# Performance work log

Hardware: AMD Instinct MI355X
Metric: run time of the kernel (lower is better)

Reference implementation:

```python
import jax, jax.numpy as jnp
import numpy as np

B, K, D, C = 16384, 8, 128, 128


def setup_inputs() -> dict:
    key = jax.random.key(0)
    k1, k2, k3, k4, k5 = jax.random.split(key, 5)
    return {
        "graph_embeddings": jax.random.normal(k1, (B, D), dtype=jnp.float32),
        "retrieval_embeddings": jax.random.normal(k2, (B, K, D), dtype=jnp.float32),
        "W_adapter": jax.random.normal(k3, (D, D), dtype=jnp.float32) / np.sqrt(D),
        "W_pred": jax.random.normal(k4, (D, C), dtype=jnp.float32) / np.sqrt(D),
        "b_pred": jnp.zeros((C,), dtype=jnp.float32),
        "labels": jax.random.randint(k5, (B, K), 0, C, dtype=jnp.int64).astype(jnp.int32),
    }


def reference(graph_embeddings, retrieval_embeddings, W_adapter, W_pred, b_pred, labels):
    # g_label = Softmax(dim=1)(graph_pred_linear(graph_embeddings))   [B, C]
    g_label = jax.nn.softmax(graph_embeddings @ W_pred + b_pred, axis=1)

    # concat_H = cat([graph_embeddings] + retrievals, -1).view(B, K+1, D)
    concat_H = jnp.concatenate([graph_embeddings[:, None, :], retrieval_embeddings], axis=1)  # [B, K+1, D]

    # adapter: bilinear attention scores, softmax over the K+1 candidates
    scores = jnp.einsum("bd,de,bme->bm", graph_embeddings, W_adapter, concat_H)  # [B, K+1]
    attention = jax.nn.softmax(scores, axis=1)

    # generic-dataset branch of the per-sample loop, vectorized:
    #   adjusted[b] = attn[b,0] * g_label[b]
    #   adjusted[b, labels[b,k]] += attn[b, k]   for k in range(K)
    # (note: faithful to the original, which indexes attention[b][k], not k+1)
    one_hot = jax.nn.one_hot(labels, C, dtype=g_label.dtype)  # [B, K, C]
    adjusted_label = attention[:, :1] * g_label + jnp.einsum("bk,bkc->bc", attention[:, :K], one_hot)
    return adjusted_label
```

## Files before the change

kernel.cpp:

```cpp
#include <hip/hip_runtime.h>


#define SB      32
#define THREADS 256

__global__ __launch_bounds__(THREADS)
void graph_retrieval_fused(const float* __restrict__ G,
                           const float* __restrict__ R,
                           const float* __restrict__ Wa,
                           const float* __restrict__ Wp,
                           const float* __restrict__ bp,
                           const int*   __restrict__ labels,
                           float* __restrict__ out)
{
    __shared__ float g_lds[SB * 128];
    __shared__ float logit_lds[SB * 132];
    __shared__ float t_lds[SB * 128];
    __shared__ float attn_lds[SB * 12];
    __shared__ float stat_m[SB], stat_iz[SB];
    __shared__ int   lab_lds[SB * 8];

    const int tid = threadIdx.x;
    const int b0  = blockIdx.x * SB;

    {
        const float4* Gv  = (const float4*)(G + (size_t)b0 * 128);
        float4*       gl4 = (float4*)g_lds;
        #pragma unroll
        for (int j = 0; j < 4; ++j)
            gl4[j * 256 + tid] = Gv[j * 256 + tid];
        lab_lds[tid] = labels[b0 * 8 + tid];
    }
    __syncthreads();

    const int c     = tid & 127;
    const int h     = tid >> 7;
    const int sbase = h * 16;

    float t_acc[16], l_acc[16];
    {
        const float bias = bp[c];
        #pragma unroll
        for (int i = 0; i < 16; ++i) { t_acc[i] = 0.f; l_acc[i] = bias; }

        for (int d0 = 0; d0 < 128; d0 += 4) {
            const float wa0 = Wa[(d0 + 0) * 128 + c];
            const float wa1 = Wa[(d0 + 1) * 128 + c];
            const float wa2 = Wa[(d0 + 2) * 128 + c];
            const float wa3 = Wa[(d0 + 3) * 128 + c];
            const float wp0 = Wp[(d0 + 0) * 128 + c];
            const float wp1 = Wp[(d0 + 1) * 128 + c];
            const float wp2 = Wp[(d0 + 2) * 128 + c];
            const float wp3 = Wp[(d0 + 3) * 128 + c];
            #pragma unroll
            for (int i = 0; i < 16; ++i) {
                const float4 g4 = *(const float4*)&g_lds[(sbase + i) * 128 + d0];
                t_acc[i] += g4.x * wa0 + g4.y * wa1 + g4.z * wa2 + g4.w * wa3;
                l_acc[i] += g4.x * wp0 + g4.y * wp1 + g4.z * wp2 + g4.w * wp3;
            }
        }

        #pragma unroll
        for (int i = 0; i < 16; ++i) {
            t_lds[(sbase + i) * 128 + c]     = t_acc[i];
            logit_lds[(sbase + i) * 132 + c] = l_acc[i];
        }
    }
    __syncthreads();

    {
        const int s = tid >> 3;
        const int p = tid & 7;
        const float* row = &logit_lds[s * 132 + p * 16];
        float mx = row[0];
        #pragma unroll
        for (int j = 1; j < 16; ++j) mx = fmaxf(mx, row[j]);
        #pragma unroll
        for (int off = 1; off < 8; off <<= 1)
            mx = fmaxf(mx, __shfl_xor(mx, off, 64));
        float sum = 0.f;
        #pragma unroll
        for (int j = 0; j < 16; ++j) sum += __expf(row[j] - mx);
        #pragma unroll
        for (int off = 1; off < 8; off <<= 1)
            sum += __shfl_xor(sum, off, 64);
        if (p == 0) { stat_m[s] = mx; stat_iz[s] = 1.f / sum; }
    }
    __syncthreads();

    {
        const int wv   = tid >> 6;
        const int lane = tid & 63;
        #pragma unroll
        for (int si = 0; si < 8; ++si) {
            const int s = wv * 8 + si;
            const float2 t2 = *(const float2*)&t_lds[s * 128 + 2 * lane];
            float sc[9];
            {
                const float2 g2 = *(const float2*)&g_lds[s * 128 + 2 * lane];
                sc[0] = t2.x * g2.x + t2.y * g2.y;
            }
            const float2* Rrow = (const float2*)(R + (size_t)(b0 + s) * 8 * 128);
            #pragma unroll
            for (int m = 1; m < 9; ++m) {
                const float2 hv = Rrow[(m - 1) * 64 + lane];
                sc[m] = t2.x * hv.x + t2.y * hv.y;
            }
            #pragma unroll
            for (int off = 32; off > 0; off >>= 1) {
                #pragma unroll
                for (int m = 0; m < 9; ++m)
                    sc[m] += __shfl_xor(sc[m], off, 64);
            }
            float mx = sc[0];
            #pragma unroll
            for (int m = 1; m < 9; ++m) mx = fmaxf(mx, sc[m]);
            float e[9], sum = 0.f;
            #pragma unroll
            for (int m = 0; m < 9; ++m) { e[m] = __expf(sc[m] - mx); sum += e[m]; }
            const float inv = 1.f / sum;
            if (lane == 0) {
                #pragma unroll
                for (int m = 0; m < 9; ++m) attn_lds[s * 12 + m] = e[m] * inv;
            }
        }
    }
    __syncthreads();

    #pragma unroll
    for (int i = 0; i < 16; ++i) {
        const int s = sbase + i;
        const float gl  = __expf(l_acc[i] - stat_m[s]) * stat_iz[s];
        float val = attn_lds[s * 12 + 0] * gl;
        #pragma unroll
        for (int k = 0; k < 8; ++k)
            val += (lab_lds[s * 8 + k] == c) ? attn_lds[s * 12 + k] : 0.f;
        out[(size_t)(b0 + s) * 128 + c] = val;
    }
}

extern "C" void kernel_launch(void* const* d_in, const int* in_sizes, int n_in,
                              void* d_out, int out_size, void* d_ws, size_t ws_size,
                              hipStream_t stream) {
    const float* G      = (const float*)d_in[0];
    const float* R      = (const float*)d_in[1];
    const float* Wa     = (const float*)d_in[2];
    const float* Wp     = (const float*)d_in[3];
    const float* bpred  = (const float*)d_in[4];
    const int*   labels = (const int*)d_in[5];
    float*       o      = (float*)d_out;

    const int B = in_sizes[0] / 128;
    dim3 grid(B / SB), block(THREADS);
    hipLaunchKernelGGL(graph_retrieval_fused, grid, block, 0, stream,
                       G, R, Wa, Wp, bpred, labels, o);
}
```

Before: 139.0 us.

## Shrink per-block sample tile to 8 and merge softmax stats into attention phase

Reduces samples per block from 32 to 8, which gives four times as many blocks, smaller LDS use and fewer accumulators per thread, aiming for higher occupancy and better latency hiding of the retrieval-embedding loads. The logit softmax statistics are now computed by each wave for its two samples with 64-lane shuffles inside the attention phase, which removes one barrier. Each wave interleaves two samples' score reductions for more instruction-level parallelism. The cost is that every block re-reads both 128x128 weight matrices for only 8 samples, so weight traffic per sample rises fourfold, mostly served from L2.

After: 137.0 us. Within noise of the previous version (-1.4%).

```diff
diff --git a/kernel.cpp b/kernel.cpp
--- a/kernel.cpp
+++ b/kernel.cpp
@@ -1,7 +1,7 @@
 #include <hip/hip_runtime.h>
 
 
-#define SB      32
+#define SB      8
 #define THREADS 256
 
 __global__ __launch_bounds__(THREADS)
@@ -14,54 +14,48 @@
                            float* __restrict__ out)
 {
     __shared__ float g_lds[SB * 128];
+    __shared__ float t_lds[SB * 128];
     __shared__ float logit_lds[SB * 132];
-    __shared__ float t_lds[SB * 128];
-    __shared__ float attn_lds[SB * 12];
+    __shared__ float attn_lds[SB * 8];
     __shared__ float stat_m[SB], stat_iz[SB];
     __shared__ int   lab_lds[SB * 8];
 
     const int tid = threadIdx.x;
     const int b0  = blockIdx.x * SB;
 
-    {
-        const float4* Gv  = (const float4*)(G + (size_t)b0 * 128);
-        float4*       gl4 = (float4*)g_lds;
-        #pragma unroll
-        for (int j = 0; j < 4; ++j)
-            gl4[j * 256 + tid] = Gv[j * 256 + tid];
-        lab_lds[tid] = labels[b0 * 8 + tid];
-    }
+    ((float4*)g_lds)[tid] = ((const float4*)(G + (size_t)b0 * 128))[tid];
+    if (tid < SB * 8) lab_lds[tid] = labels[b0 * 8 + tid];
     __syncthreads();
 
     const int c     = tid & 127;
     const int h     = tid >> 7;
-    const int sbase = h * 16;
+    const int sbase = h * 4;
 
-    float t_acc[16], l_acc[16];
+    float t_acc[4], l_acc[4];
     {
         const float bias = bp[c];
         #pragma unroll
-        for (int i = 0; i < 16; ++i) { t_acc[i] = 0.f; l_acc[i] = bias; }
+        for (int i = 0; i < 4; ++i) { t_acc[i] = 0.f; l_acc[i] = bias; }
 
-        for (int d0 = 0; d0 < 128; d0 += 4) {
-            const float wa0 = Wa[(d0 + 0) * 128 + c];
-            const float wa1 = Wa[(d0 + 1) * 128 + c];
-            const float wa2 = Wa[(d0 + 2) * 128 + c];
-            const float wa3 = Wa[(d0 + 3) * 128 + c];
-            const float wp0 = Wp[(d0 + 0) * 128 + c];
-            const float wp1 = Wp[(d0 + 1) * 128 + c];
-            const float wp2 = Wp[(d0 + 2) * 128 + c];
-            const float wp3 = Wp[(d0 + 3) * 128 + c];
+        for (int d0 = 0; d0 < 128; d0 += 8) {
+            float wa[8], wp8[8];
             #pragma unroll
-            for (int i = 0; i < 16; ++i) {
-                const float4 g4 = *(const float4*)&g_lds[(sbase + i) * 128 + d0];
-                t_acc[i] += g4.x * wa0 + g4.y * wa1 + g4.z * wa2 + g4.w * wa3;
-                l_acc[i] += g4.x * wp0 + g4.y * wp1 + g4.z * wp2 + g4.w * wp3;
+            for (int j = 0; j < 8; ++j) {
+                wa[j]  = Wa[(d0 + j) * 128 + c];
+                wp8[j] = Wp[(d0 + j) * 128 + c];
+            }
+            #pragma unroll
+            for (int i = 0; i < 4; ++i) {
+                const float4 ga = *(const float4*)&g_lds[(sbase + i) * 128 + d0];
+                const float4 gb = *(const float4*)&g_lds[(sbase + i) * 128 + d0 + 4];
+                t_acc[i] += ga.x * wa[0] + ga.y * wa[1] + ga.z * wa[2] + ga.w * wa[3]
+                          + gb.x * wa[4] + gb.y * wa[5] + gb.z * wa[6] + gb.w * wa[7];
+                l_acc[i] += ga.x * wp8[0] + ga.y * wp8[1] + ga.z * wp8[2] + ga.w * wp8[3]
+                          + gb.x * wp8[4] + gb.y * wp8[5] + gb.z * wp8[6] + gb.w * wp8[7];
             }
         }
-
         #pragma unroll
-        for (int i = 0; i < 16; ++i) {
+        for (int i = 0; i < 4; ++i) {
             t_lds[(sbase + i) * 128 + c]     = t_acc[i];
             logit_lds[(sbase + i) * 132 + c] = l_acc[i];
         }
@@ -69,72 +63,84 @@
     __syncthreads();
 
     {
-        const int s = tid >> 3;
-        const int p = tid & 7;
-        const float* row = &logit_lds[s * 132 + p * 16];
-        float mx = row[0];
-        #pragma unroll
-        for (int j = 1; j < 16; ++j) mx = fmaxf(mx, row[j]);
-        #pragma unroll
-        for (int off = 1; off < 8; off <<= 1)
-            mx = fmaxf(mx, __shfl_xor(mx, off, 64));
-        float sum = 0.f;
-        #pragma unroll
-        for (int j = 0; j < 16; ++j) sum += __expf(row[j] - mx);
-        #pragma unroll
-        for (int off = 1; off < 8; off <<= 1)
-            sum += __shfl_xor(sum, off, 64);
-        if (p == 0) { stat_m[s] = mx; stat_iz[s] = 1.f / sum; }
-    }
-    __syncthreads();
-
-    {
         const int wv   = tid >> 6;
         const int lane = tid & 63;
+        const int s0   = wv * 2;
+
+        const float2 e0 = *(const float2*)&logit_lds[s0 * 132 + 2 * lane];
+        const float2 e1 = *(const float2*)&logit_lds[(s0 + 1) * 132 + 2 * lane];
+        float m0 = fmaxf(e0.x, e0.y), m1 = fmaxf(e1.x, e1.y);
         #pragma unroll
-        for (int si = 0; si < 8; ++si) {
-            const int s = wv * 8 + si;
-            const float2 t2 = *(const float2*)&t_lds[s * 128 + 2 * lane];
-            float sc[9];
-            {
-                const float2 g2 = *(const float2*)&g_lds[s * 128 + 2 * lane];
-                sc[0] = t2.x * g2.x + t2.y * g2.y;
-            }
-            const float2* Rrow = (const float2*)(R + (size_t)(b0 + s) * 8 * 128);
+        for (int off = 32; off > 0; off >>= 1) {
+            m0 = fmaxf(m0, __shfl_xor(m0, off, 64));
+            m1 = fmaxf(m1, __shfl_xor(m1, off, 64));
+        }
+        float z0 = __expf(e0.x - m0) + __expf(e0.y - m0);
+        float z1 = __expf(e1.x - m1) + __expf(e1.y - m1);
+        #pragma unroll
+        for (int off = 32; off > 0; off >>= 1) {
+            z0 += __shfl_xor(z0, off, 64);
+            z1 += __shfl_xor(z1, off, 64);
+        }
+        if (lane == 0) {
+            stat_m[s0]      = m0;  stat_iz[s0]      = 1.f / z0;
+            stat_m[s0 + 1]  = m1;  stat_iz[s0 + 1]  = 1.f / z1;
+        }
+
+        float scA[9], scB[9];
+        {
+            const float2 tA = *(const float2*)&t_lds[s0 * 128 + 2 * lane];
+            const float2 tB = *(const float2*)&t_lds[(s0 + 1) * 128 + 2 * lane];
+            const float2 gA = *(const float2*)&g_lds[s0 * 128 + 2 * lane];
+            const float2 gB = *(const float2*)&g_lds[(s0 + 1) * 128 + 2 * lane];
+            scA[0] = tA.x * gA.x + tA.y * gA.y;
+            scB[0] = tB.x * gB.x + tB.y * gB.y;
+            const float2* RrA = (const float2*)(R + (size_t)(b0 + s0) * 8 * 128);
+            const float2* RrB = (const float2*)(R + (size_t)(b0 + s0 + 1) * 8 * 128);
             #pragma unroll
             for (int m = 1; m < 9; ++m) {
-                const float2 hv = Rrow[(m - 1) * 64 + lane];
-                sc[m] = t2.x * hv.x + t2.y * hv.y;
+                const float2 ra = RrA[(m - 1) * 64 + lane];
+                const float2 rb = RrB[(m - 1) * 64 + lane];
+                scA[m] = tA.x * ra.x + tA.y * ra.y;
+                scB[m] = tB.x * rb.x + tB.y * rb.y;
             }
+        }
+        #pragma unroll
+        for (int off = 32; off > 0; off >>= 1) {
             #pragma unroll
-            for (int off = 32; off > 0; off >>= 1) {
-                #pragma unroll
-                for (int m = 0; m < 9; ++m)
-                    sc[m] += __shfl_xor(sc[m], off, 64);
+            for (int m = 0; m < 9; ++m) {
+                scA[m] += __shfl_xor(scA[m], off, 64);
+                scB[m] += __shfl_xor(scB[m], off, 64);
             }
-            float mx = sc[0];
+        }
+        float mxA = scA[0], mxB = scB[0];
+        #pragma unroll
+        for (int m = 1; m < 9; ++m) { mxA = fmaxf(mxA, scA[m]); mxB = fmaxf(mxB, scB[m]); }
+        float eA[9], eB[9], sA = 0.f, sB = 0.f;
+        #pragma unroll
+        for (int m = 0; m < 9; ++m) {
+            eA[m] = __expf(scA[m] - mxA); sA += eA[m];
+            eB[m] = __expf(scB[m] - mxB); sB += eB[m];
+        }
+        const float iA = 1.f / sA, iB = 1.f / sB;
+        if (lane == 0) {
             #pragma unroll
-            for (int m = 1; m < 9; ++m) mx = fmaxf(mx, sc[m]);
-            float e[9], sum = 0.f;
-            #pragma unroll
-            for (int m = 0; m < 9; ++m) { e[m] = __expf(sc[m] - mx); sum += e[m]; }
-            const float inv = 1.f / sum;
-            if (lane == 0) {
-                #pragma unroll
-                for (int m = 0; m < 9; ++m) attn_lds[s * 12 + m] = e[m] * inv;
+            for (int m = 0; m < 8; ++m) {
+                attn_lds[s0 * 8 + m]       = eA[m] * iA;
+                attn_lds[(s0 + 1) * 8 + m] = eB[m] * iB;
             }
         }
     }
     __syncthreads();
 
     #pragma unroll
-    for (int i = 0; i < 16; ++i) {
+    for (int i = 0; i < 4; ++i) {
         const int s = sbase + i;
-        const float gl  = __expf(l_acc[i] - stat_m[s]) * stat_iz[s];
-        float val = attn_lds[s * 12 + 0] * gl;
+        const float gl = __expf(l_acc[i] - stat_m[s]) * stat_iz[s];
+        float val = attn_lds[s * 8 + 0] * gl;
         #pragma unroll
         for (int k = 0; k < 8; ++k)
-            val += (lab_lds[s * 8 + k] == c) ? attn_lds[s * 12 + k] : 0.f;
+            val += (lab_lds[s * 8 + k] == c) ? attn_lds[s * 8 + k] : 0.f;
         out[(size_t)(b0 + s) * 128 + c] = val;
     }
 }
```

## Compute G×[Wa|Wp] with split-bf16 MFMA and prepacked weight fragments

Applied to the files above, without the earlier changes.

Replaces the scalar FP32 projection loop with bf16 MFMA 16x16x32 instructions, using a hi/lo bf16 split (three MFMAs per tile) to approximate FP32 accuracy. A small pre-kernel packs Wa and Wp into MFMA B-fragment layout in the workspace on every call. Also halves rows per block to 16, pads LDS rows, and fuses the logit softmax stats with the attention-score phase to remove one barrier. This trades some precision (truncated bf16 split) and an extra launch for less scalar FMA work.

Measured after the change: 120.1 us. -13.6%, faster.

```diff
diff --git a/kernel.cpp b/kernel.cpp
--- a/kernel.cpp
+++ b/kernel.cpp
@@ -1,141 +1,226 @@
 #include <hip/hip_runtime.h>
 
 
-#define SB      32
+#define SB      16
 #define THREADS 256
 
-__global__ __launch_bounds__(THREADS)
+typedef __attribute__((ext_vector_type(8))) short bfrag_t;
+typedef __attribute__((ext_vector_type(4))) float facc_t;
+
+__device__ __forceinline__ unsigned short bf16_hi_trunc(float f) {
+    return (unsigned short)(__builtin_bit_cast(unsigned int, f) >> 16);
+}
+__device__ __forceinline__ float bf16_up(unsigned short h) {
+    return __builtin_bit_cast(float, ((unsigned int)h) << 16);
+}
+
+__global__ __launch_bounds__(256)
+void pack_w_kernel(const float* __restrict__ Wa, const float* __restrict__ Wp,
+                   unsigned short* __restrict__ w_hi, unsigned short* __restrict__ w_lo) {
+    const int t    = blockIdx.x * 256 + threadIdx.x;
+    const int nt   = t >> 8;
+    const int kk   = (t >> 6) & 3;
+    const int lane = t & 63;
+    const int n    = nt * 16 + (lane & 15);
+    const int kb   = kk * 32 + (lane >> 4) * 8;
+    const float* W = (n < 128) ? Wa : Wp;
+    const int col  = n & 127;
+    unsigned int h[4], l[4];
+    #pragma unroll
+    for (int i = 0; i < 4; ++i) {
+        const float v0 = W[(kb + 2 * i) * 128 + col];
+        const float v1 = W[(kb + 2 * i + 1) * 128 + col];
+        const unsigned short h0 = bf16_hi_trunc(v0), h1 = bf16_hi_trunc(v1);
+        const unsigned short l0 = bf16_hi_trunc(v0 - bf16_up(h0));
+        const unsigned short l1 = bf16_hi_trunc(v1 - bf16_up(h1));
+        h[i] = (unsigned int)h0 | ((unsigned int)h1 << 16);
+        l[i] = (unsigned int)l0 | ((unsigned int)l1 << 16);
+    }
+    ((uint4*)w_hi)[t] = make_uint4(h[0], h[1], h[2], h[3]);
+    ((uint4*)w_lo)[t] = make_uint4(l[0], l[1], l[2], l[3]);
+}
+
+__global__ __launch_bounds__(THREADS, 4)
 void graph_retrieval_fused(const float* __restrict__ G,
                            const float* __restrict__ R,
-                           const float* __restrict__ Wa,
-                           const float* __restrict__ Wp,
+                           const unsigned short* __restrict__ w_hi,
+                           const unsigned short* __restrict__ w_lo,
                            const float* __restrict__ bp,
                            const int*   __restrict__ labels,
                            float* __restrict__ out)
 {
-    __shared__ float g_lds[SB * 128];
+    __shared__ float g_lds[SB * 132];
+    __shared__ float t_lds[SB * 132];
     __shared__ float logit_lds[SB * 132];
-    __shared__ float t_lds[SB * 128];
-    __shared__ float attn_lds[SB * 12];
+    __shared__ float attn_lds[SB * 8];
     __shared__ float stat_m[SB], stat_iz[SB];
     __shared__ int   lab_lds[SB * 8];
 
-    const int tid = threadIdx.x;
-    const int b0  = blockIdx.x * SB;
-
-    {
-        const float4* Gv  = (const float4*)(G + (size_t)b0 * 128);
-        float4*       gl4 = (float4*)g_lds;
-        #pragma unroll
-        for (int j = 0; j < 4; ++j)
-            gl4[j * 256 + tid] = Gv[j * 256 + tid];
-        lab_lds[tid] = labels[b0 * 8 + tid];
+    const int tid  = threadIdx.x;
+    const int b0   = blockIdx.x * SB;
+    const int wv   = tid >> 6;
+    const int lane = tid & 63;
+
+    {
+        const float4* Gv = (const float4*)(G + (size_t)b0 * 128);
+        #pragma unroll
+        for (int rpt = 0; rpt < 2; ++rpt) {
+            const int idx = rpt * 256 + tid;
+            const int row = idx >> 5, j = idx & 31;
+            ((float4*)g_lds)[row * 33 + j] = Gv[idx];
+        }
+        if (tid < SB * 8) lab_lds[tid] = labels[b0 * 8 + tid];
     }
     __syncthreads();
 
-    const int c     = tid & 127;
-    const int h     = tid >> 7;
-    const int sbase = h * 16;
-
-    float t_acc[16], l_acc[16];
-    {
-        const float bias = bp[c];
-        #pragma unroll
-        for (int i = 0; i < 16; ++i) { t_acc[i] = 0.f; l_acc[i] = bias; }
-
-        for (int d0 = 0; d0 < 128; d0 += 4) {
-            const float wa0 = Wa[(d0 + 0) * 128 + c];
-            const float wa1 = Wa[(d0 + 1) * 128 + c];
-            const float wa2 = Wa[(d0 + 2) * 128 + c];
-            const float wa3 = Wa[(d0 + 3) * 128 + c];
-            const float wp0 = Wp[(d0 + 0) * 128 + c];
-            const float wp1 = Wp[(d0 + 1) * 128 + c];
-            const float wp2 = Wp[(d0 + 2) * 128 + c];
-            const float wp3 = Wp[(d0 + 3) * 128 + c];
-            #pragma unroll
-            for (int i = 0; i < 16; ++i) {
-                const float4 g4 = *(const float4*)&g_lds[(sbase + i) * 128 + d0];
-                t_acc[i] += g4.x * wa0 + g4.y * wa1 + g4.z * wa2 + g4.w * wa3;
-                l_acc[i] += g4.x * wp0 + g4.y * wp1 + g4.z * wp2 + g4.w * wp3;
-            }
-        }
-
-        #pragma unroll
-        for (int i = 0; i < 16; ++i) {
-            t_lds[(sbase + i) * 128 + c]     = t_acc[i];
-            logit_lds[(sbase + i) * 132 + c] = l_acc[i];
+    {
+        const int arow = lane & 15;
+        const int kch  = lane >> 4;
+        bfrag_t a_hi[4], a_lo[4];
+        #pragma unroll
+        for (int kk = 0; kk < 4; ++kk) {
+            const float* src = &g_lds[arow * 132 + kk * 32 + kch * 8];
+            const float4 f0 = *(const float4*)src;
+            const float4 f1 = *(const float4*)(src + 4);
+            const float f[8] = {f0.x, f0.y, f0.z, f0.w, f1.x, f1.y, f1.z, f1.w};
+            #pragma unroll
+            for (int i = 0; i < 8; ++i) {
+                const unsigned short hb = bf16_hi_trunc(f[i]);
+                a_hi[kk][i] = (short)hb;
+                a_lo[kk][i] = (short)bf16_hi_trunc(f[i] - bf16_up(hb));
+            }
+        }
+
+        facc_t acc[4] = {{0.f,0.f,0.f,0.f},{0.f,0.f,0.f,0.f},
+                         {0.f,0.f,0.f,0.f},{0.f,0.f,0.f,0.f}};
+        #pragma unroll
+        for (int p = 0; p < 4; ++p) {
+            const int nt = wv * 4 + p;
+            #pragma unroll
+            for (int kk = 0; kk < 4; ++kk) {
+                const int idx = (nt * 4 + kk) * 64 + lane;
+                const bfrag_t bh = ((const bfrag_t*)w_hi)[idx];
+                const bfrag_t bl = ((const bfrag_t*)w_lo)[idx];
+                acc[p] = __builtin_amdgcn_mfma_f32_16x16x32_bf16(a_hi[kk], bh, acc[p], 0, 0, 0);
+                acc[p] = __builtin_amdgcn_mfma_f32_16x16x32_bf16(a_lo[kk], bh, acc[p], 0, 0, 0);
+                acc[p] = __builtin_amdgcn_mfma_f32_16x16x32_bf16(a_hi[kk], bl, acc[p], 0, 0, 0);
+            }
+        }
+
+        const int crow = (lane >> 4) * 4;
+        #pragma unroll
+        for (int p = 0; p < 4; ++p) {
+            const int coll = p * 16 + (lane & 15);
+            if (wv < 2) {
+                const int c_t = wv * 64 + coll;
+                #pragma unroll
+                for (int j = 0; j < 4; ++j)
+                    t_lds[(crow + j) * 132 + c_t] = acc[p][j];
+            } else {
+                const int c_l = (wv - 2) * 64 + coll;
+                const float bias = bp[c_l];
+                #pragma unroll
+                for (int j = 0; j < 4; ++j)
+                    logit_lds[(crow + j) * 132 + c_l] = acc[p][j] + bias;
+            }
         }
     }
     __syncthreads();
 
     {
-        const int s = tid >> 3;
-        const int p = tid & 7;
-        const float* row = &logit_lds[s * 132 + p * 16];
-        float mx = row[0];
-        #pragma unroll
-        for (int j = 1; j < 16; ++j) mx = fmaxf(mx, row[j]);
-        #pragma unroll
-        for (int off = 1; off < 8; off <<= 1)
-            mx = fmaxf(mx, __shfl_xor(mx, off, 64));
-        float sum = 0.f;
-        #pragma unroll
-        for (int j = 0; j < 16; ++j) sum += __expf(row[j] - mx);
-        #pragma unroll
-        for (int off = 1; off < 8; off <<= 1)
-            sum += __shfl_xor(sum, off, 64);
-        if (p == 0) { stat_m[s] = mx; stat_iz[s] = 1.f / sum; }
-    }
-    __syncthreads();
-
-    {
-        const int wv   = tid >> 6;
-        const int lane = tid & 63;
-        #pragma unroll
-        for (int si = 0; si < 8; ++si) {
-            const int s = wv * 8 + si;
-            const float2 t2 = *(const float2*)&t_lds[s * 128 + 2 * lane];
-            float sc[9];
-            {
-                const float2 g2 = *(const float2*)&g_lds[s * 128 + 2 * lane];
-                sc[0] = t2.x * g2.x + t2.y * g2.y;
-            }
-            const float2* Rrow = (const float2*)(R + (size_t)(b0 + s) * 8 * 128);
+        const int s0 = wv * 4;
+
+        float mx[4], zs[4];
+        float2 ev[4];
+        #pragma unroll
+        for (int q = 0; q < 4; ++q) {
+            ev[q] = *(const float2*)&logit_lds[(s0 + q) * 132 + 2 * lane];
+            mx[q] = fmaxf(ev[q].x, ev[q].y);
+        }
+        #pragma unroll
+        for (int off = 32; off > 0; off >>= 1)
+            #pragma unroll
+            for (int q = 0; q < 4; ++q)
+                mx[q] = fmaxf(mx[q], __shfl_xor(mx[q], off, 64));
+        #pragma unroll
+        for (int q = 0; q < 4; ++q)
+            zs[q] = __expf(ev[q].x - mx[q]) + __expf(ev[q].y - mx[q]);
+        #pragma unroll
+        for (int off = 32; off > 0; off >>= 1)
+            #pragma unroll
+            for (int q = 0; q < 4; ++q)
+                zs[q] += __shfl_xor(zs[q], off, 64);
+        if (lane == 0) {
+            #pragma unroll
+            for (int q = 0; q < 4; ++q) {
+                stat_m[s0 + q]  = mx[q];
+                stat_iz[s0 + q] = 1.f / zs[q];
+            }
+        }
+
+        float sc[4][9];
+        #pragma unroll
+        for (int q = 0; q < 4; ++q) {
+            const int s = s0 + q;
+            const float2 t2 = *(const float2*)&t_lds[s * 132 + 2 * lane];
+            const float2 g2 = *(const float2*)&g_lds[s * 132 + 2 * lane];
+            sc[q][0] = t2.x * g2.x + t2.y * g2.y;
+            const float2* Rr = (const float2*)(R + (size_t)(b0 + s) * 1024);
             #pragma unroll
             for (int m = 1; m < 9; ++m) {
-                const float2 hv = Rrow[(m - 1) * 64 + lane];
-                sc[m] = t2.x * hv.x + t2.y * hv.y;
-            }
-            #pragma unroll
-            for (int off = 32; off > 0; off >>= 1) {
+                const float2 r2 = Rr[(m - 1) * 64 + lane];
+                sc[q][m] = t2.x * r2.x + t2.y * r2.y;
+            }
+        }
+        #pragma unroll
+        for (int off = 32; off > 0; off >>= 1)
+            #pragma unroll
+            for (int q = 0; q < 4; ++q)
                 #pragma unroll
                 for (int m = 0; m < 9; ++m)
-                    sc[m] += __shfl_xor(sc[m], off, 64);
-            }
-            float mx = sc[0];
-            #pragma unroll
-            for (int m = 1; m < 9; ++m) mx = fmaxf(mx, sc[m]);
+                    sc[q][m] += __shfl_xor(sc[q][m], off, 64);
+
+        #pragma unroll
+        for (int q = 0; q < 4; ++q) {
+            float m9 = sc[q][0];
+            #pragma unroll
+            for (int m = 1; m < 9; ++m) m9 = fmaxf(m9, sc[q][m]);
             float e[9], sum = 0.f;
             #pragma unroll
-            for (int m = 0; m < 9; ++m) { e[m] = __expf(sc[m] - mx); sum += e[m]; }
+            for (int m = 0; m < 9; ++m) { e[m] = __expf(sc[q][m] - m9); sum += e[m]; }
             const float inv = 1.f / sum;
             if (lane == 0) {
                 #pragma unroll
-                for (int m = 0; m < 9; ++m) attn_lds[s * 12 + m] = e[m] * inv;
+                for (int m = 0; m < 8; ++m)
+                    attn_lds[(s0 + q) * 8 + m] = e[m] * inv;
             }
         }
     }
     __syncthreads();
 
-    #pragma unroll
-    for (int i = 0; i < 16; ++i) {
-        const int s = sbase + i;
-        const float gl  = __expf(l_acc[i] - stat_m[s]) * stat_iz[s];
-        float val = attn_lds[s * 12 + 0] * gl;
-        #pragma unroll
-        for (int k = 0; k < 8; ++k)
-            val += (lab_lds[s * 8 + k] == c) ? attn_lds[s * 12 + k] : 0.f;
-        out[(size_t)(b0 + s) * 128 + c] = val;
+    {
+        const int c  = tid & 127;
+        const int hh = tid >> 7;
+        #pragma unroll
+        for (int i = 0; i < 8; ++i) {
+            const int s = hh * 8 + i;
+            const float lg = logit_lds[s * 132 + c];
+            const float gl = __expf(lg - stat_m[s]) * stat_iz[s];
+            const int4   la = *(const int4*)&lab_lds[s * 8];
+            const int4   lb = *(const int4*)&lab_lds[s * 8 + 4];
+            const float4 a0 = *(const float4*)&attn_lds[s * 8];
+            const float4 a1 = *(const float4*)&attn_lds[s * 8 + 4];
+            float val = a0.x * gl;
+            val += (la.x == c) ? a0.x : 0.f;
+            val += (la.y == c) ? a0.y : 0.f;
+            val += (la.z == c) ? a0.z : 0.f;
+            val += (la.w == c) ? a0.w : 0.f;
+            val += (lb.x == c) ? a1.x : 0.f;
+            val += (lb.y == c) ? a1.y : 0.f;
+            val += (lb.z == c) ? a1.z : 0.f;
+            val += (lb.w == c) ? a1.w : 0.f;
+            out[(size_t)(b0 + s) * 128 + c] = val;
+        }
     }
 }
 
@@ -150,8 +235,13 @@
     const int*   labels = (const int*)d_in[5];
     float*       o      = (float*)d_out;
 
+    unsigned short* w_hi = (unsigned short*)d_ws;
+    unsigned short* w_lo = w_hi + 4096 * 8;
+
+    hipLaunchKernelGGL(pack_w_kernel, dim3(16), dim3(256), 0, stream,
+                       Wa, Wp, w_hi, w_lo);
+
     const int B = in_sizes[0] / 128;
-    dim3 grid(B / SB), block(THREADS);
-    hipLaunchKernelGGL(graph_retrieval_fused, grid, block, 0, stream,
-                       G, R, Wa, Wp, bpred, labels, o);
-}
+    hipLaunchKernelGGL(graph_retrieval_fused, dim3(B / SB), dim3(THREADS), 0, stream,
+                       G, R, w_hi, w_lo, bpred, labels, o);
+}
```
